# Kernel optimization log

Hardware: AMD Instinct MI355X
Metric: run time of the kernel (lower is better)

## Reference

```python
import jax, jax.numpy as jnp
import numpy as np


def _maxpool2x2(x):
    # x: [B, C, H, W] -> [B, C, H//2, W//2], 2x2 max pool stride 2
    B, C, H, W = x.shape
    return x.reshape(B, C, H // 2, 2, W // 2, 2).max(axis=(3, 5))


def setup_inputs() -> dict:
    key = jax.random.key(0)
    ks = jax.random.split(key, 5)
    C = 64
    B, H, W = 16, 64, 64
    x = jax.random.normal(ks[0], (B, C, H, W), dtype=jnp.float32)
    s = 0.05
    W_theta = jax.random.normal(ks[1], (C // 8, C), dtype=jnp.float32) * s
    W_phi = jax.random.normal(ks[2], (C // 8, C), dtype=jnp.float32) * s
    W_g = jax.random.normal(ks[3], (C // 2, C), dtype=jnp.float32) * s
    W_attn = jax.random.normal(ks[4], (C, C // 2), dtype=jnp.float32) * s
    sigma = jnp.zeros((1,), dtype=jnp.float32)
    return {"x": x, "W_theta": W_theta, "W_phi": W_phi, "W_g": W_g,
            "W_attn": W_attn, "sigma": sigma}


def reference(x, W_theta, W_phi, W_g, W_attn, sigma):
    B, C, H, W = x.shape
    HW = H * W
    # 1x1 convs are channel GEMMs
    theta = jnp.einsum('oc,bchw->bohw', W_theta, x).reshape(B, C // 8, HW)
    phi = jnp.einsum('oc,bchw->bohw', W_phi, x)
    phi = _maxpool2x2(phi).reshape(B, C // 8, HW // 4)
    # attn: [B, HW, HW//4]
    attn = jax.nn.softmax(jnp.einsum('bcq,bck->bqk', theta, phi), axis=-1)
    g = jnp.einsum('oc,bchw->bohw', W_g, x)
    g = _maxpool2x2(g).reshape(B, C // 2, HW // 4)
    # attn_g: [B, C//2, HW]
    attn_g = jnp.einsum('bck,bqk->bcq', g, attn).reshape(B, C // 2, H, W)
    attn_g = jnp.einsum('oc,bchw->bohw', W_attn, attn_g)
    return x + sigma[0] * attn_g
```

## Files before the change

kernel.cpp:

```cpp
#include <hip/hip_runtime.h>
#include <math.h>

#define B_ 16
#define C_ 64
#define HW_ 4096
#define PHW_ 1024

typedef __attribute__((ext_vector_type(8))) short bf8;
typedef __attribute__((ext_vector_type(16))) float fv16;

union FU { bf8 v; unsigned u[4]; };

__device__ inline unsigned short f2bf(float f) {
    unsigned u = __float_as_uint(f);
    return (unsigned short)((u + 0x7FFFu + ((u >> 16) & 1u)) >> 16);
}
__device__ inline unsigned packbf(float a, float b) {
    return (unsigned)f2bf(a) | ((unsigned)f2bf(b) << 16);
}
__device__ inline unsigned packtr(float a, float b) {
    return (__float_as_uint(a) >> 16) | (__float_as_uint(b) & 0xFFFF0000u);
}

__global__ __launch_bounds__(256) void conv_stage(
    const float* __restrict__ x,
    const float* __restrict__ Wt,
    const float* __restrict__ Wp,
    const float* __restrict__ Wg,
    float* __restrict__ theta,
    unsigned short* __restrict__ phi_pack,
    unsigned short* __restrict__ g_pack)
{
    __shared__ float sx[64][128];
    __shared__ float pool2[40][33];

    const int t  = threadIdx.x;
    const int b  = blockIdx.x >> 5;
    const int h2 = blockIdx.x & 31;

    const float* xbase = x + (size_t)b * C_ * HW_ + h2 * 128;
    for (int f = t; f < 2048; f += 256) {
        int c = f >> 5, j4 = f & 31;
        *(float4*)&sx[c][j4 * 4] = *(const float4*)&xbase[(size_t)c * HW_ + j4 * 4];
    }
    __syncthreads();

    const int wv   = __builtin_amdgcn_readfirstlane(t >> 6);
    const int lane = t & 63;
    const int chbase = wv * 12;

    const float* wrow[12];
#pragma unroll
    for (int j = 0; j < 12; j++) {
        int gch = chbase + j;
        wrow[j] = (gch < 8) ? (Wt + gch * 64)
                : (gch < 16) ? (Wp + (gch - 8) * 64)
                             : (Wg + (gch - 16) * 64);
    }

    float acc[12][2];
#pragma unroll
    for (int j = 0; j < 12; j++) { acc[j][0] = 0.f; acc[j][1] = 0.f; }

    for (int c = 0; c < 64; c++) {
        float2 xv = *(const float2*)&sx[c][2 * lane];
#pragma unroll
        for (int j = 0; j < 12; j++) {
            float w = wrow[j][c];
            acc[j][0] += w * xv.x;
            acc[j][1] += w * xv.y;
        }
    }

    if (wv == 0) {
        float* tp = theta + (size_t)b * 8 * HW_ + h2 * 128 + 2 * lane;
#pragma unroll
        for (int j = 0; j < 8; j++)
            *(float2*)&tp[(size_t)j * HW_] = make_float2(acc[j][0], acc[j][1]);
    }

#pragma unroll
    for (int j = 0; j < 12; j++) {
        int gch = chbase + j;
        if (gch >= 8) {
            float hm = fmaxf(acc[j][0], acc[j][1]);
            float pm = fmaxf(hm, __shfl_xor(hm, 32));
            if (lane < 32) pool2[gch - 8][lane] = pm;
        }
    }
    __syncthreads();

    if (t < 64) {
        unsigned u0 = 0, u1 = 0, u2 = 0, u3 = 0;
        if (t < 32) {
            float v[8];
#pragma unroll
            for (int j = 0; j < 8; j++) v[j] = pool2[j][t];
            u0 = packbf(v[0], v[1]); u1 = packbf(v[2], v[3]);
            u2 = packbf(v[4], v[5]); u3 = packbf(v[6], v[7]);
        }
        uint4 pkt = make_uint4(u0, u1, u2, u3);
        *(uint4*)(phi_pack + ((size_t)((b * 32 + h2) * 64 + t)) * 8) = pkt;
    } else if (t < 192) {
        const int tt  = t - 64;
        const int ktl = tt >> 6;
        const int ln  = tt & 63;
        const int c   = ln & 31;
        const int hh  = ln >> 5;
        float v[8];
#pragma unroll
        for (int j = 0; j < 8; j++) v[j] = pool2[8 + c][ktl * 16 + hh * 8 + j];
        uint4 pkt = make_uint4(packbf(v[0], v[1]), packbf(v[2], v[3]),
                               packbf(v[4], v[5]), packbf(v[6], v[7]));
        *(uint4*)(g_pack + ((size_t)((b * 64 + h2 * 2 + ktl) * 64 + ln)) * 8) = pkt;
    }
}

__global__ __launch_bounds__(256, 4) void attn_mfma(
    const float* __restrict__ theta_g,
    const unsigned short* __restrict__ phi_pack,
    const unsigned short* __restrict__ g_pack,
    const float* __restrict__ Wa,
    const float* __restrict__ x,
    const float* __restrict__ sigma,
    float* __restrict__ out)
{
    __shared__ float comb[4][64][17];

    const int t = threadIdx.x, wave = t >> 6, lane = t & 63;
    const int lo = lane & 31, hi = lane >> 5;
    const int qtile = blockIdx.x * 2 + (wave >> 1);
    const int khalf = wave & 1;
    const int b = qtile >> 7, qt = qtile & 127;
    const int qg = qt * 32 + lo;

    FU tb; tb.u[0] = tb.u[1] = tb.u[2] = tb.u[3] = 0;
    if (hi == 0) {
        const float LOG2E = 1.4426950408889634f;
        float tv[8];
#pragma unroll
        for (int j = 0; j < 8; j++)
            tv[j] = theta_g[(((size_t)b * 8 + j) << 12) + qg] * LOG2E;
        tb.u[0] = packbf(tv[0], tv[1]); tb.u[1] = packbf(tv[2], tv[3]);
        tb.u[2] = packbf(tv[4], tv[5]); tb.u[3] = packbf(tv[6], tv[7]);
    }

    fv16 zf, acc;
#pragma unroll
    for (int r = 0; r < 16; r++) { zf[r] = 0.f; acc[r] = 0.f; }
    float ps = 0.f;

    const int kt0 = khalf * 16;
    const unsigned short* phip = phi_pack + ((size_t)((b * 32 + kt0) * 64 + lane)) * 8;
    const unsigned short* gp   = g_pack   + ((size_t)((b * 64 + kt0 * 2) * 64 + lane)) * 8;

#pragma unroll 2
    for (int i = 0; i < 16; i++) {
        FU pa, ga0, ga1;
        pa.v  = *(const bf8*)(phip + (size_t)i * 512);
        ga0.v = *(const bf8*)(gp + (size_t)i * 1024);
        ga1.v = *(const bf8*)(gp + (size_t)i * 1024 + 512);
        fv16 s = __builtin_amdgcn_mfma_f32_32x32x16_bf16(pa.v, tb.v, zf, 0, 0, 0);

        {
            unsigned pk[4], qk[4];
#pragma unroll
            for (int u = 0; u < 4; u++) {
                float p0 = __builtin_amdgcn_exp2f(s[2 * u]);
                float p1 = __builtin_amdgcn_exp2f(s[2 * u + 1]);
                ps += p0 + p1;
                pk[u] = packtr(p0, p1);
            }
#pragma unroll
            for (int u = 0; u < 4; u++) qk[u] = (unsigned)__shfl_xor((int)pk[u], 32);
            FU pb;
            pb.u[0] = hi ? qk[2] : pk[0]; pb.u[1] = hi ? qk[3] : pk[1];
            pb.u[2] = hi ? pk[2] : qk[0]; pb.u[3] = hi ? pk[3] : qk[1];
            acc = __builtin_amdgcn_mfma_f32_32x32x16_bf16(ga0.v, pb.v, acc, 0, 0, 0);
        }
        {
            unsigned pk[4], qk[4];
#pragma unroll
            for (int u = 0; u < 4; u++) {
                float p0 = __builtin_amdgcn_exp2f(s[8 + 2 * u]);
                float p1 = __builtin_amdgcn_exp2f(s[9 + 2 * u]);
                ps += p0 + p1;
                pk[u] = packtr(p0, p1);
            }
#pragma unroll
            for (int u = 0; u < 4; u++) qk[u] = (unsigned)__shfl_xor((int)pk[u], 32);
            FU pb;
            pb.u[0] = hi ? qk[2] : pk[0]; pb.u[1] = hi ? qk[3] : pk[1];
            pb.u[2] = hi ? pk[2] : qk[0]; pb.u[3] = hi ? pk[3] : qk[1];
            acc = __builtin_amdgcn_mfma_f32_32x32x16_bf16(ga1.v, pb.v, acc, 0, 0, 0);
        }
    }

#pragma unroll
    for (int r = 0; r < 16; r++) comb[wave][lane][r] = acc[r];
    comb[wave][lane][16] = ps;
    __syncthreads();
    const int pw = wave ^ 1;
#pragma unroll
    for (int r = 0; r < 16; r++) acc[r] += comb[pw][lane][r];
    ps += comb[pw][lane][16];

    float lsum = ps + __shfl_xor(ps, 32);
    float inv = 1.f / lsum;

    float on[16];
#pragma unroll
    for (int r = 0; r < 16; r++) on[r] = acc[r] * inv;
    unsigned pk[8], qk[8];
#pragma unroll
    for (int i = 0; i < 8; i++) pk[i] = packtr(on[2 * i], on[2 * i + 1]);
#pragma unroll
    for (int i = 0; i < 8; i++) qk[i] = (unsigned)__shfl_xor((int)pk[i], 32);
    FU ob0, ob1;
    ob0.u[0] = hi ? qk[2] : pk[0]; ob0.u[1] = hi ? qk[3] : pk[1];
    ob0.u[2] = hi ? pk[2] : qk[0]; ob0.u[3] = hi ? pk[3] : qk[1];
    ob1.u[0] = hi ? qk[6] : pk[4]; ob1.u[1] = hi ? qk[7] : pk[5];
    ob1.u[2] = hi ? pk[6] : qk[4]; ob1.u[3] = hi ? pk[7] : qk[5];

    FU wa0, wa1;
    {
        const float* wr = Wa + (khalf * 32 + lo) * 32;
#pragma unroll
        for (int ktw = 0; ktw < 2; ktw++) {
            float w8[8];
#pragma unroll
            for (int j = 0; j < 8; j++) w8[j] = wr[ktw * 16 + hi * 8 + j];
            FU f;
            f.u[0] = packbf(w8[0], w8[1]); f.u[1] = packbf(w8[2], w8[3]);
            f.u[2] = packbf(w8[4], w8[5]); f.u[3] = packbf(w8[6], w8[7]);
            if (ktw == 0) wa0 = f; else wa1 = f;
        }
    }
    fv16 d2 = __builtin_amdgcn_mfma_f32_32x32x16_bf16(wa0.v, ob0.v, zf, 0, 0, 0);
    d2 = __builtin_amdgcn_mfma_f32_32x32x16_bf16(wa1.v, ob1.v, d2, 0, 0, 0);

    const float sig = sigma[0];
#pragma unroll
    for (int r = 0; r < 16; r++) {
        int row = (r & 3) + ((r >> 2) << 3) + (hi << 2);
        int o = khalf * 32 + row;
        size_t idx = (((size_t)b * 64 + o) << 12) + qg;
        out[idx] = x[idx] + sig * d2[r];
    }
}

extern "C" void kernel_launch(void* const* d_in, const int* in_sizes, int n_in,
                              void* d_out, int out_size, void* d_ws, size_t ws_size,
                              hipStream_t stream) {
    const float* x     = (const float*)d_in[0];
    const float* Wt    = (const float*)d_in[1];
    const float* Wp    = (const float*)d_in[2];
    const float* Wg    = (const float*)d_in[3];
    const float* Wa    = (const float*)d_in[4];
    const float* sigma = (const float*)d_in[5];
    float* out = (float*)d_out;

    float* theta = (float*)d_ws;
    unsigned short* phi_pack = (unsigned short*)(theta + (size_t)B_ * 8 * HW_);
    unsigned short* g_pack   = phi_pack + (size_t)B_ * 32 * 64 * 8;

    conv_stage<<<512, 256, 0, stream>>>(x, Wt, Wp, Wg, theta, phi_pack, g_pack);
    attn_mfma<<<1024, 256, 0, stream>>>(theta, phi_pack, g_pack, Wa, x, sigma, out);
}
```

Measured before the change: 108.0 us.

## Compute 1x1 conv projections in conv_stage with bf16 MFMA instead of scalar FMAs

Replaces the scalar per-lane FMA loop that computed the theta/phi/g channel projections with two 32x32x16 bf16 MFMAs per 16-channel slice. Weights and x are packed to bf16, and the 2x2 pooling is rebuilt around the MFMA output layout via lane shuffles and a two-half shared buffer. This lowers conv-stage ALU work and weight reloads, but theta is now computed with bf16 inputs, which reduces precision.

Result: faster. 99.73 us (median of 2 runs) (-7.7%).

```diff
diff --git a/kernel.cpp b/kernel.cpp
--- a/kernel.cpp
+++ b/kernel.cpp
@@ -32,7 +32,7 @@
     unsigned short* __restrict__ g_pack)
 {
     __shared__ float sx[64][128];
-    __shared__ float pool2[40][33];
+    __shared__ float poolh[2][40][33];
 
     const int t  = threadIdx.x;
     const int b  = blockIdx.x >> 5;
@@ -43,49 +43,73 @@
         int c = f >> 5, j4 = f & 31;
         *(float4*)&sx[c][j4 * 4] = *(const float4*)&xbase[(size_t)c * HW_ + j4 * 4];
     }
+
+    const int wv = t >> 6, lane = t & 63, lo = lane & 31, hi = lane >> 5;
+
+    FU wa[2][4];
+    {
+        const float* r0 = (lo < 8)  ? (Wt + lo * 64)
+                        : (lo < 16) ? (Wp + (lo - 8) * 64)
+                                    : (Wg + (lo - 16) * 64);
+        const float* r1 = Wg + ((lo < 16) ? (16 + lo) : 0) * 64;
+#pragma unroll
+        for (int cs = 0; cs < 4; cs++) {
+            const int c0 = cs * 16 + hi * 8;
+            float4 a0 = *(const float4*)&r0[c0];
+            float4 b0 = *(const float4*)&r0[c0 + 4];
+            wa[0][cs].u[0] = packbf(a0.x, a0.y); wa[0][cs].u[1] = packbf(a0.z, a0.w);
+            wa[0][cs].u[2] = packbf(b0.x, b0.y); wa[0][cs].u[3] = packbf(b0.z, b0.w);
+            float4 a1 = *(const float4*)&r1[c0];
+            float4 b1 = *(const float4*)&r1[c0 + 4];
+            if (lo >= 16) { a1 = make_float4(0.f,0.f,0.f,0.f); b1 = make_float4(0.f,0.f,0.f,0.f); }
+            wa[1][cs].u[0] = packbf(a1.x, a1.y); wa[1][cs].u[1] = packbf(a1.z, a1.w);
+            wa[1][cs].u[2] = packbf(b1.x, b1.y); wa[1][cs].u[3] = packbf(b1.z, b1.w);
+        }
+    }
     __syncthreads();
 
-    const int wv   = __builtin_amdgcn_readfirstlane(t >> 6);
-    const int lane = t & 63;
-    const int chbase = wv * 12;
-
-    const float* wrow[12];
-#pragma unroll
-    for (int j = 0; j < 12; j++) {
-        int gch = chbase + j;
-        wrow[j] = (gch < 8) ? (Wt + gch * 64)
-                : (gch < 16) ? (Wp + (gch - 8) * 64)
-                             : (Wg + (gch - 16) * 64);
-    }
-
-    float acc[12][2];
-#pragma unroll
-    for (int j = 0; j < 12; j++) { acc[j][0] = 0.f; acc[j][1] = 0.f; }
-
-    for (int c = 0; c < 64; c++) {
-        float2 xv = *(const float2*)&sx[c][2 * lane];
-#pragma unroll
-        for (int j = 0; j < 12; j++) {
-            float w = wrow[j][c];
-            acc[j][0] += w * xv.x;
-            acc[j][1] += w * xv.y;
-        }
-    }
-
-    if (wv == 0) {
-        float* tp = theta + (size_t)b * 8 * HW_ + h2 * 128 + 2 * lane;
-#pragma unroll
-        for (int j = 0; j < 8; j++)
-            *(float2*)&tp[(size_t)j * HW_] = make_float2(acc[j][0], acc[j][1]);
-    }
-
-#pragma unroll
-    for (int j = 0; j < 12; j++) {
-        int gch = chbase + j;
-        if (gch >= 8) {
-            float hm = fmaxf(acc[j][0], acc[j][1]);
-            float pm = fmaxf(hm, __shfl_xor(hm, 32));
-            if (lane < 32) pool2[gch - 8][lane] = pm;
+    fv16 acc0, acc1;
+#pragma unroll
+    for (int r = 0; r < 16; r++) { acc0[r] = 0.f; acc1[r] = 0.f; }
+
+    const int px = wv * 32 + lo;
+#pragma unroll
+    for (int cs = 0; cs < 4; cs++) {
+        const float* sp = &sx[cs * 16 + hi * 8][px];
+        float v[8];
+#pragma unroll
+        for (int j = 0; j < 8; j++) v[j] = sp[j * 128];
+        FU xb;
+        xb.u[0] = packbf(v[0], v[1]); xb.u[1] = packbf(v[2], v[3]);
+        xb.u[2] = packbf(v[4], v[5]); xb.u[3] = packbf(v[6], v[7]);
+        acc0 = __builtin_amdgcn_mfma_f32_32x32x16_bf16(wa[0][cs].v, xb.v, acc0, 0, 0, 0);
+        acc1 = __builtin_amdgcn_mfma_f32_32x32x16_bf16(wa[1][cs].v, xb.v, acc1, 0, 0, 0);
+    }
+
+    {
+        float* tp = theta + (size_t)b * 8 * HW_ + h2 * 128 + px;
+#pragma unroll
+        for (int r = 0; r < 4; r++) tp[(size_t)(r + 4 * hi) * HW_] = acc0[r];
+    }
+
+    const int prow = wv >> 1;
+    const int pcol = (wv & 1) * 16 + (lo >> 1);
+#pragma unroll
+    for (int r = 4; r < 16; r++) {
+        float vv = acc0[r];
+        float hm = fmaxf(vv, __shfl_xor(vv, 1));
+        if ((lane & 1) == 0) {
+            int m = (r & 3) + 8 * (r >> 2) + 4 * hi;
+            poolh[prow][m - 8][pcol] = hm;
+        }
+    }
+#pragma unroll
+    for (int r = 0; r < 8; r++) {
+        float vv = acc1[r];
+        float hm = fmaxf(vv, __shfl_xor(vv, 1));
+        if ((lane & 1) == 0) {
+            int m1 = (r & 3) + 8 * (r >> 2) + 4 * hi;
+            poolh[prow][24 + m1][pcol] = hm;
         }
     }
     __syncthreads();
@@ -95,7 +119,8 @@
         if (t < 32) {
             float v[8];
 #pragma unroll
-            for (int j = 0; j < 8; j++) v[j] = pool2[j][t];
+            for (int j = 0; j < 8; j++)
+                v[j] = fmaxf(poolh[0][j][t], poolh[1][j][t]);
             u0 = packbf(v[0], v[1]); u1 = packbf(v[2], v[3]);
             u2 = packbf(v[4], v[5]); u3 = packbf(v[6], v[7]);
         }
@@ -109,7 +134,10 @@
         const int hh  = ln >> 5;
         float v[8];
 #pragma unroll
-        for (int j = 0; j < 8; j++) v[j] = pool2[8 + c][ktl * 16 + hh * 8 + j];
+        for (int j = 0; j < 8; j++) {
+            int p = ktl * 16 + hh * 8 + j;
+            v[j] = fmaxf(poolh[0][8 + c][p], poolh[1][8 + c][p]);
+        }
         uint4 pkt = make_uint4(packbf(v[0], v[1]), packbf(v[2], v[3]),
                                packbf(v[4], v[5]), packbf(v[6], v[7]));
         *(uint4*)(g_pack + ((size_t)((b * 64 + h2 * 2 + ktl) * 64 + ln)) * 8) = pkt;
```
